# Performance work log

Measured on AMD Instinct MI355X. Metric: run time of the kernel, lower is better.

Reference implementation:

```python
import jax, jax.numpy as jnp
import numpy as np

N_NODES = 10000
N_EDGES = 160000
C = 16        # num_feature_channels
C2 = 8        # output channels per irrep per head (C/2)
HID = 64      # radial_network_hidden_units
NH = 2        # num_attention_heads
NG = 16       # graphs in batch
F_IN = 64     # num_features
F_OUT = 32    # number_of_output_features
HEAD_TYPES = ("normal", "inverse")  # invariant_dictionary
IRREP_SLICES = ((0, 1), (1, 4), (4, 9))  # l=0,1,2 blocks of the SH dim


def _sph_harm(r):
    """Component-normalized real spherical harmonics l=0..2 for unit vectors r [E,3] -> [E,9]."""
    x, y, z = r[:, 0], r[:, 1], r[:, 2]
    c3 = 1.7320508   # sqrt(3)
    c15 = 3.8729833  # sqrt(15)
    l0 = jnp.ones_like(x)[:, None]
    l1 = c3 * r
    l2 = jnp.stack([
        c15 * x * y,
        c15 * y * z,
        1.1180340 * (2.0 * z * z - x * x - y * y),  # sqrt(5)/2
        c15 * x * z,
        1.9364917 * (x * x - y * y),                 # sqrt(15)/2
    ], axis=-1)
    return jnp.concatenate([l0, l1, l2], axis=-1)


def setup_inputs() -> dict:
    key = jax.random.key(0)
    ks = jax.random.split(key, 16)
    node_features = jax.random.normal(ks[0], (N_NODES, F_IN), jnp.float32)
    pos = jax.random.normal(ks[1], (N_NODES, 3), jnp.float32)
    src = jax.random.randint(ks[2], (N_EDGES,), 0, N_NODES)
    off = jax.random.randint(ks[3], (N_EDGES,), 1, N_NODES)  # avoid self-loops (d=0)
    tgt = (src + off) % N_NODES
    edge_index = jnp.stack([src, tgt], axis=0)
    batch = jnp.sort(jax.random.randint(ks[4], (N_NODES,), 0, NG))
    s = lambda k, shape, fan: (jax.random.normal(k, shape, jnp.float32) / np.sqrt(fan)).astype(jnp.float32)
    return dict(
        node_features=node_features, pos=pos,
        W_embed=s(ks[5], (F_IN, C), F_IN), b_embed=jnp.zeros((C,), jnp.float32),
        Wq=s(ks[6], (NH, C, C), C), Wk=s(ks[7], (NH, C, C), C),
        W1=s(ks[8], (NH, 1, HID), 1), b1=jnp.zeros((NH, HID), jnp.float32),
        Wa=s(ks[9], (NH, HID), HID), Wv=s(ks[10], (NH, HID, C * 3), HID),
        Wo=s(ks[11], (NH, 3, C, C2), C),
        Wproj=s(ks[12], (NH * C2, F_OUT), NH * C2), bproj=jnp.zeros((F_OUT,), jnp.float32),
        edge_index=edge_index, batch=batch,
    )


def _forward(node_features, pos, W_embed, b_embed, Wq, Wk, W1, b1, Wa, Wv, Wo,
             Wproj, bproj, edge_index, batch):
    src, tgt = edge_index[0], edge_index[1]
    rel = pos[tgt] - pos[src]                       # [E,3]
    dist = jnp.linalg.norm(rel, axis=-1, keepdims=True)  # [E,1]
    rhat = rel / dist
    Y = _sph_harm(rhat)                             # [E,9]
    x = node_features @ W_embed + b_embed          # [N,C] scalar (0e) features
    xs = x[src]                                     # [E,C]
    inv_sqrt_c = 1.0 / np.sqrt(C)
    head_outs = []
    for h in range(NH):
        d_feat = dist if HEAD_TYPES[h] == "normal" else dist ** -2  # [E,1]
        hid = jax.nn.relu(d_feat @ W1[h] + b1[h])   # [E,HID] radial network
        att_bias = hid @ Wa[h]                      # [E]
        wv = (hid @ Wv[h]).reshape(-1, C, 3)        # [E,C,3] per-(channel,l) radial weights
        q = x @ Wq[h]
        k = x @ Wk[h]
        logit = jnp.sum(q[tgt] * k[src], axis=-1) * inv_sqrt_c + att_bias  # [E]
        # segment softmax over incoming edges of each target node
        m = jax.ops.segment_max(logit, tgt, num_segments=N_NODES)
        e = jnp.exp(logit - m[tgt])
        z = jax.ops.segment_sum(e, tgt, num_segments=N_NODES)
        alpha = e / z[tgt]                          # [E]
        # expand per-l weights to per-m: dims (1,3,5)
        wv_m = jnp.repeat(wv, np.array([1, 3, 5]), axis=2, total_repeat_length=9)  # [E,C,9]
        msg = (alpha[:, None, None] * wv_m) * xs[:, :, None] * Y[:, None, :]       # [E,C,9]
        node_out = jax.ops.segment_sum(msg, tgt, num_segments=N_NODES)             # [N,C,9]
        parts = [jnp.einsum('ncm,co->nom', node_out[:, :, s0:s1], Wo[h, li]).reshape(N_NODES, -1)
                 for li, (s0, s1) in enumerate(IRREP_SLICES)]
        head_outs.append(jnp.concatenate(parts, axis=-1))  # [N, C2*9]
    feat = jnp.concatenate(head_outs, axis=-1)              # [N, NH*C2*9]
    pooled = jax.ops.segment_sum(feat, batch, num_segments=NG)  # [NG, NH*C2*9]
    # equivariant Linear -> F_OUT x 0e: only scalar (l=0) components map to scalars
    blk = C2 * 9
    scal = jnp.concatenate([pooled[:, h * blk: h * blk + C2] for h in range(NH)], axis=-1)  # [NG, NH*C2]
    return scal @ Wproj + bproj                             # [NG, F_OUT]


def reference(node_features, pos, W_embed, b_embed, Wq, Wk, W1, b1, Wa, Wv, Wo,
              Wproj, bproj, edge_index, batch):
    return _forward(node_features, pos, W_embed, b_embed, Wq, Wk, W1, b1, Wa, Wv,
                    Wo, Wproj, bproj, edge_index, batch)
```

## Files before the change

### kernel.cpp

```cpp
#include <hip/hip_runtime.h>
#include <math.h>

#define NN 10000
#define NE 160000
#define CAP 96

__global__ __launch_bounds__(256) void k_xqk(const float* __restrict__ nf,
        const float* __restrict__ We, const float* __restrict__ be,
        const float* __restrict__ Wq, const float* __restrict__ Wk,
        float* __restrict__ x, float* __restrict__ q, float* __restrict__ k,
        int* __restrict__ zeroReg) {
    int t = threadIdx.x;
    int gid = blockIdx.x * 256 + t;
    if (gid < 10256) zeroReg[gid] = 0;
    __shared__ float sWe[64 * 16];
    __shared__ float sWq[2 * 16 * 16];
    __shared__ float sWk[2 * 16 * 16];
    __shared__ float sNF[16 * 64];
    __shared__ float sX[16 * 16];
    for (int i = t; i < 1024; i += 256) sWe[i] = We[i];
    for (int i = t; i < 512; i += 256) { sWq[i] = Wq[i]; sWk[i] = Wk[i]; }
    int nodeBase = blockIdx.x * 16;
    for (int i = t; i < 1024; i += 256) {
        int n = nodeBase + (i >> 6);
        sNF[i] = (n < NN) ? nf[n * 64 + (i & 63)] : 0.0f;
    }
    __syncthreads();
    int ln = t >> 4, c = t & 15;
    int n = nodeBase + ln;
    float acc = be[c];
    #pragma unroll 16
    for (int j = 0; j < 64; ++j) acc = fmaf(sNF[ln * 64 + j], sWe[j * 16 + c], acc);
    sX[ln * 16 + c] = acc;
    __syncthreads();
    if (n < NN) {
        x[n * 16 + c] = acc;
        #pragma unroll
        for (int h = 0; h < 2; ++h) {
            float aq = 0.0f, ak = 0.0f;
            #pragma unroll
            for (int j = 0; j < 16; ++j) {
                float xv = sX[ln * 16 + j];
                aq = fmaf(xv, sWq[(h * 16 + j) * 16 + c], aq);
                ak = fmaf(xv, sWk[(h * 16 + j) * 16 + c], ak);
            }
            q[(n * 2 + h) * 16 + c] = aq;
            k[(n * 2 + h) * 16 + c] = ak;
        }
    }
}

__global__ __launch_bounds__(256) void k_edge(const float* __restrict__ pos,
        const int* __restrict__ ei,
        const float* __restrict__ q, const float* __restrict__ k,
        const float* __restrict__ W1, const float* __restrict__ b1,
        const float* __restrict__ Wa, const float* __restrict__ Wv,
        const float* __restrict__ x, int* __restrict__ deg,
        float* __restrict__ lgp, float* __restrict__ wxs) {
    __shared__ float sW1[128], sB1[128], sWa[128];
    __shared__ float sV[2048];
    int t0 = threadIdx.x;
    if (t0 < 128) { sW1[t0] = W1[t0]; sB1[t0] = b1[t0]; sWa[t0] = Wa[t0]; }
    for (int i = t0; i < 2048; i += 256) {
        int h = i >> 10, j = (i >> 4) & 63, c = i & 15;
        sV[i] = Wv[(h * 64 + j) * 48 + 3 * c];
    }
    __syncthreads();
    int e = blockIdx.x * 256 + t0;
    if (e >= NE) return;
    int s = ei[e], t = ei[NE + e];
    int p = atomicAdd(&deg[t], 1);
    bool ok = (p < CAP);
    size_t slot = (size_t)t * CAP + p;
    float dx = pos[t * 3 + 0] - pos[s * 3 + 0];
    float dy = pos[t * 3 + 1] - pos[s * 3 + 1];
    float dz = pos[t * 3 + 2] - pos[s * 3 + 2];
    float d = sqrtf(dx * dx + dy * dy + dz * dz);
    float fh[2] = { d, 1.0f / (d * d) };
    const float4* qt = (const float4*)(q + (size_t)t * 32);
    const float4* ks = (const float4*)(k + (size_t)s * 32);
    const float4* xp = (const float4*)(x + (size_t)s * 16);
    float4 xs[4] = { xp[0], xp[1], xp[2], xp[3] };
    float L2v[2];
    float4* wp = (float4*)(wxs + slot * 32);
    #pragma unroll
    for (int h = 0; h < 2; ++h) {
        float4 a0 = qt[h * 4 + 0], a1 = qt[h * 4 + 1], a2 = qt[h * 4 + 2], a3 = qt[h * 4 + 3];
        float4 b0 = ks[h * 4 + 0], c1 = ks[h * 4 + 1], c2 = ks[h * 4 + 2], c3 = ks[h * 4 + 3];
        float dot = a0.x * b0.x + a0.y * b0.y + a0.z * b0.z + a0.w * b0.w
                  + a1.x * c1.x + a1.y * c1.y + a1.z * c1.z + a1.w * c1.w
                  + a2.x * c2.x + a2.y * c2.y + a2.z * c2.z + a2.w * c2.w
                  + a3.x * c3.x + a3.y * c3.y + a3.z * c3.z + a3.w * c3.w;
        float f = fh[h];
        float att = 0.0f;
        float acc[16];
        #pragma unroll
        for (int c = 0; c < 16; ++c) acc[c] = 0.0f;
        const float4* vp = (const float4*)(sV + h * 1024);
        for (int j = 0; j < 64; ++j) {
            float hj = fmaxf(fmaf(f, sW1[h * 64 + j], sB1[h * 64 + j]), 0.0f);
            att = fmaf(hj, sWa[h * 64 + j], att);
            float4 v0 = vp[j * 4 + 0], v1 = vp[j * 4 + 1], v2 = vp[j * 4 + 2], v3 = vp[j * 4 + 3];
            acc[0]  = fmaf(hj, v0.x, acc[0]);  acc[1]  = fmaf(hj, v0.y, acc[1]);
            acc[2]  = fmaf(hj, v0.z, acc[2]);  acc[3]  = fmaf(hj, v0.w, acc[3]);
            acc[4]  = fmaf(hj, v1.x, acc[4]);  acc[5]  = fmaf(hj, v1.y, acc[5]);
            acc[6]  = fmaf(hj, v1.z, acc[6]);  acc[7]  = fmaf(hj, v1.w, acc[7]);
            acc[8]  = fmaf(hj, v2.x, acc[8]);  acc[9]  = fmaf(hj, v2.y, acc[9]);
            acc[10] = fmaf(hj, v2.z, acc[10]); acc[11] = fmaf(hj, v2.w, acc[11]);
            acc[12] = fmaf(hj, v3.x, acc[12]); acc[13] = fmaf(hj, v3.y, acc[13]);
            acc[14] = fmaf(hj, v3.z, acc[14]); acc[15] = fmaf(hj, v3.w, acc[15]);
        }
        L2v[h] = fmaf(dot, 0.25f, att);
        if (ok) {
            wp[h * 4 + 0] = make_float4(acc[0] * xs[0].x, acc[1] * xs[0].y, acc[2] * xs[0].z, acc[3] * xs[0].w);
            wp[h * 4 + 1] = make_float4(acc[4] * xs[1].x, acc[5] * xs[1].y, acc[6] * xs[1].z, acc[7] * xs[1].w);
            wp[h * 4 + 2] = make_float4(acc[8] * xs[2].x, acc[9] * xs[2].y, acc[10] * xs[2].z, acc[11] * xs[2].w);
            wp[h * 4 + 3] = make_float4(acc[12] * xs[3].x, acc[13] * xs[3].y, acc[14] * xs[3].z, acc[15] * xs[3].w);
        }
    }
    if (ok) *(float2*)(lgp + slot * 2) = make_float2(L2v[0], L2v[1]);
}

__global__ __launch_bounds__(256) void k_gather(const int* __restrict__ deg,
        const float* __restrict__ lgp, const float* __restrict__ wxs,
        const float* __restrict__ Wo, float* __restrict__ feat) {
    __shared__ float sWo[256];
    __shared__ float sUn[4][16];
    int t0 = threadIdx.x;
    sWo[t0] = Wo[(t0 >> 7) * 384 + (t0 & 127)];
    __syncthreads();
    int wv = t0 >> 6;
    int lane = t0 & 63;
    int pid = blockIdx.x * 4 + wv;
    int n = pid >> 1, h = pid & 1;
    int dg = min(deg[n], CAP);
    int g = lane >> 4, c = lane & 15;
    float m = -INFINITY, z = 0.0f, u = 0.0f;
    const float* lgb = lgp + (size_t)n * (CAP * 2) + h;
    const float* wxb = wxs + (size_t)n * (CAP * 32) + h * 16 + c;
    for (int i = g; i < dg; i += 4) {
        float L  = lgb[i * 2];
        float wx = wxb[(size_t)i * 32];
        float nm = fmaxf(m, L);
        float sc = __expf(m - nm);
        float w  = __expf(L - nm);
        u = fmaf(u, sc, w * wx);
        z = fmaf(z, sc, w);
        m = nm;
    }
    #pragma unroll
    for (int off = 16; off <= 32; off <<= 1) {
        float mo = __shfl_xor(m, off, 64);
        float zo = __shfl_xor(z, off, 64);
        float uo = __shfl_xor(u, off, 64);
        float nm = fmaxf(m, mo);
        float a = __expf(m - nm), b = __expf(mo - nm);
        u = u * a + uo * b;
        z = z * a + zo * b;
        m = nm;
    }
    float un = (z > 0.0f) ? u / z : 0.0f;
    sUn[wv][c] = un;
    if (lane < 8) {
        float o_acc = 0.0f;
        #pragma unroll
        for (int cc = 0; cc < 16; ++cc)
            o_acc = fmaf(sUn[wv][cc], sWo[h * 128 + cc * 8 + lane], o_acc);
        feat[n * 16 + h * 8 + lane] = o_acc;
    }
}

__global__ __launch_bounds__(256) void k_pool(const float* __restrict__ feat,
        const int* __restrict__ batch, float* __restrict__ pooled) {
    __shared__ float sP[256];
    int t = threadIdx.x;
    sP[t] = 0.0f;
    __syncthreads();
    for (int i = blockIdx.x * 256 + t; i < NN * 16; i += 40 * 256) {
        int n = i >> 4, c = i & 15;
        atomicAdd(&sP[batch[n] * 16 + c], feat[i]);
    }
    __syncthreads();
    atomicAdd(&pooled[t], sP[t]);
}

__global__ __launch_bounds__(512) void k_final(const float* __restrict__ pooled,
        const float* __restrict__ Wproj, const float* __restrict__ bproj,
        float* __restrict__ out) {
    int t = threadIdx.x;
    int g = t >> 5, fo = t & 31;
    float acc = bproj[fo];
    #pragma unroll
    for (int j = 0; j < 16; ++j) acc = fmaf(pooled[g * 16 + j], Wproj[j * 32 + fo], acc);
    out[g * 32 + fo] = acc;
}

extern "C" void kernel_launch(void* const* d_in, const int* in_sizes, int n_in,
                              void* d_out, int out_size, void* d_ws, size_t ws_size,
                              hipStream_t stream) {
    const float* nf    = (const float*)d_in[0];
    const float* pos   = (const float*)d_in[1];
    const float* We    = (const float*)d_in[2];
    const float* be    = (const float*)d_in[3];
    const float* Wq    = (const float*)d_in[4];
    const float* Wk    = (const float*)d_in[5];
    const float* W1    = (const float*)d_in[6];
    const float* b1    = (const float*)d_in[7];
    const float* Wa    = (const float*)d_in[8];
    const float* Wv    = (const float*)d_in[9];
    const float* Wo    = (const float*)d_in[10];
    const float* Wproj = (const float*)d_in[11];
    const float* bproj = (const float*)d_in[12];
    const int*   ei    = (const int*)d_in[13];
    const int*   batch = (const int*)d_in[14];
    float* out = (float*)d_out;
    (void)in_sizes; (void)n_in; (void)out_size; (void)ws_size;

    float* ws     = (float*)d_ws;
    float* x      = ws;
    float* q      = x + 160000;
    float* k      = q + 320000;
    float* feat   = k + 320000;
    float* pooled = feat + 160000;
    int*   deg    = (int*)(pooled + 256);
    float* lgp    = (float*)(deg + 10000);
    float* wxs    = lgp + (size_t)NN * CAP * 2;

    hipLaunchKernelGGL(k_xqk,    dim3(625),  dim3(256), 0, stream, nf, We, be, Wq, Wk, x, q, k, (int*)pooled);
    hipLaunchKernelGGL(k_edge,   dim3(625),  dim3(256), 0, stream, pos, ei, q, k, W1, b1, Wa, Wv, x, deg, lgp, wxs);
    hipLaunchKernelGGL(k_gather, dim3(5000), dim3(256), 0, stream, deg, lgp, wxs, Wo, feat);
    hipLaunchKernelGGL(k_pool,   dim3(40),   dim3(256), 0, stream, feat, batch, pooled);
    hipLaunchKernelGGL(k_final,  dim3(1),    dim3(512), 0, stream, pooled, Wproj, bproj, out);
}
```

Measured before the change: 139.7 us.

## Apply Wo projection per edge before softmax gather to halve scattered payload

Because Wo is linear, it is applied to each edge's weighted value vector in the edge kernel, so each slot stores 8 projected values per head instead of 16. The gather kernel then reads half as much data and skips its shared-memory Wo step. The Wv column extraction moves into a precompute in the first kernel, and the edge kernel now reads weights from global memory instead of shared memory. This trades extra per-edge FMAs and uncached-in-LDS weight loads for lower memory traffic, and adds -inf guards in the online softmax.

```diff
diff --git a/kernel.cpp b/kernel.cpp
--- a/kernel.cpp
+++ b/kernel.cpp
@@ -8,11 +8,18 @@
 __global__ __launch_bounds__(256) void k_xqk(const float* __restrict__ nf,
         const float* __restrict__ We, const float* __restrict__ be,
         const float* __restrict__ Wq, const float* __restrict__ Wk,
+        const float* __restrict__ Wv,
         float* __restrict__ x, float* __restrict__ q, float* __restrict__ k,
-        int* __restrict__ zeroReg) {
+        int* __restrict__ zeroReg, float* __restrict__ vC) {
     int t = threadIdx.x;
     int gid = blockIdx.x * 256 + t;
     if (gid < 10256) zeroReg[gid] = 0;
+    if (blockIdx.x == 0) {
+        for (int i = t; i < 2048; i += 256) {
+            int h = i >> 10, j = (i >> 4) & 63, c = i & 15;
+            vC[i] = Wv[(h * 64 + j) * 48 + 3 * c];
+        }
+    }
     __shared__ float sWe[64 * 16];
     __shared__ float sWq[2 * 16 * 16];
     __shared__ float sWk[2 * 16 * 16];
@@ -54,19 +61,11 @@
         const int* __restrict__ ei,
         const float* __restrict__ q, const float* __restrict__ k,
         const float* __restrict__ W1, const float* __restrict__ b1,
-        const float* __restrict__ Wa, const float* __restrict__ Wv,
+        const float* __restrict__ Wa, const float* __restrict__ vC,
+        const float* __restrict__ Wo,
         const float* __restrict__ x, int* __restrict__ deg,
-        float* __restrict__ lgp, float* __restrict__ wxs) {
-    __shared__ float sW1[128], sB1[128], sWa[128];
-    __shared__ float sV[2048];
-    int t0 = threadIdx.x;
-    if (t0 < 128) { sW1[t0] = W1[t0]; sB1[t0] = b1[t0]; sWa[t0] = Wa[t0]; }
-    for (int i = t0; i < 2048; i += 256) {
-        int h = i >> 10, j = (i >> 4) & 63, c = i & 15;
-        sV[i] = Wv[(h * 64 + j) * 48 + 3 * c];
-    }
-    __syncthreads();
-    int e = blockIdx.x * 256 + t0;
+        float* __restrict__ lgp, float* __restrict__ gws) {
+    int e = blockIdx.x * 256 + threadIdx.x;
     if (e >= NE) return;
     int s = ei[e], t = ei[NE + e];
     int p = atomicAdd(&deg[t], 1);
@@ -77,16 +76,17 @@
     float dz = pos[t * 3 + 2] - pos[s * 3 + 2];
     float d = sqrtf(dx * dx + dy * dy + dz * dz);
     float fh[2] = { d, 1.0f / (d * d) };
-    const float4* qt = (const float4*)(q + (size_t)t * 32);
-    const float4* ks = (const float4*)(k + (size_t)s * 32);
     const float4* xp = (const float4*)(x + (size_t)s * 16);
-    float4 xs[4] = { xp[0], xp[1], xp[2], xp[3] };
+    float4 xs0 = xp[0], xs1 = xp[1], xs2 = xp[2], xs3 = xp[3];
+    float xf[16] = { xs0.x, xs0.y, xs0.z, xs0.w, xs1.x, xs1.y, xs1.z, xs1.w,
+                     xs2.x, xs2.y, xs2.z, xs2.w, xs3.x, xs3.y, xs3.z, xs3.w };
     float L2v[2];
-    float4* wp = (float4*)(wxs + slot * 32);
     #pragma unroll
     for (int h = 0; h < 2; ++h) {
-        float4 a0 = qt[h * 4 + 0], a1 = qt[h * 4 + 1], a2 = qt[h * 4 + 2], a3 = qt[h * 4 + 3];
-        float4 b0 = ks[h * 4 + 0], c1 = ks[h * 4 + 1], c2 = ks[h * 4 + 2], c3 = ks[h * 4 + 3];
+        const float4* qt = (const float4*)(q + (size_t)t * 32 + h * 16);
+        const float4* ks = (const float4*)(k + (size_t)s * 32 + h * 16);
+        float4 a0 = qt[0], a1 = qt[1], a2 = qt[2], a3 = qt[3];
+        float4 b0 = ks[0], c1 = ks[1], c2 = ks[2], c3 = ks[3];
         float dot = a0.x * b0.x + a0.y * b0.y + a0.z * b0.z + a0.w * b0.w
                   + a1.x * c1.x + a1.y * c1.y + a1.z * c1.z + a1.w * c1.w
                   + a2.x * c2.x + a2.y * c2.y + a2.z * c2.z + a2.w * c2.w
@@ -96,78 +96,75 @@
         float acc[16];
         #pragma unroll
         for (int c = 0; c < 16; ++c) acc[c] = 0.0f;
-        const float4* vp = (const float4*)(sV + h * 1024);
+        const float* w1b = W1 + h * 64;
+        const float* b1b = b1 + h * 64;
+        const float* wab = Wa + h * 64;
+        const float* vcb = vC + h * 1024;
+        #pragma unroll 8
         for (int j = 0; j < 64; ++j) {
-            float hj = fmaxf(fmaf(f, sW1[h * 64 + j], sB1[h * 64 + j]), 0.0f);
-            att = fmaf(hj, sWa[h * 64 + j], att);
-            float4 v0 = vp[j * 4 + 0], v1 = vp[j * 4 + 1], v2 = vp[j * 4 + 2], v3 = vp[j * 4 + 3];
-            acc[0]  = fmaf(hj, v0.x, acc[0]);  acc[1]  = fmaf(hj, v0.y, acc[1]);
-            acc[2]  = fmaf(hj, v0.z, acc[2]);  acc[3]  = fmaf(hj, v0.w, acc[3]);
-            acc[4]  = fmaf(hj, v1.x, acc[4]);  acc[5]  = fmaf(hj, v1.y, acc[5]);
-            acc[6]  = fmaf(hj, v1.z, acc[6]);  acc[7]  = fmaf(hj, v1.w, acc[7]);
-            acc[8]  = fmaf(hj, v2.x, acc[8]);  acc[9]  = fmaf(hj, v2.y, acc[9]);
-            acc[10] = fmaf(hj, v2.z, acc[10]); acc[11] = fmaf(hj, v2.w, acc[11]);
-            acc[12] = fmaf(hj, v3.x, acc[12]); acc[13] = fmaf(hj, v3.y, acc[13]);
-            acc[14] = fmaf(hj, v3.z, acc[14]); acc[15] = fmaf(hj, v3.w, acc[15]);
+            float hid = fmaxf(fmaf(f, w1b[j], b1b[j]), 0.0f);
+            att = fmaf(hid, wab[j], att);
+            #pragma unroll
+            for (int c = 0; c < 16; ++c)
+                acc[c] = fmaf(hid, vcb[j * 16 + c], acc[c]);
         }
         L2v[h] = fmaf(dot, 0.25f, att);
+        float g[8];
+        #pragma unroll
+        for (int o = 0; o < 8; ++o) g[o] = 0.0f;
+        const float* wob = Wo + h * 384;
+        #pragma unroll
+        for (int c = 0; c < 16; ++c) {
+            float axc = acc[c] * xf[c];
+            #pragma unroll
+            for (int o = 0; o < 8; ++o) g[o] = fmaf(axc, wob[c * 8 + o], g[o]);
+        }
         if (ok) {
-            wp[h * 4 + 0] = make_float4(acc[0] * xs[0].x, acc[1] * xs[0].y, acc[2] * xs[0].z, acc[3] * xs[0].w);
-            wp[h * 4 + 1] = make_float4(acc[4] * xs[1].x, acc[5] * xs[1].y, acc[6] * xs[1].z, acc[7] * xs[1].w);
-            wp[h * 4 + 2] = make_float4(acc[8] * xs[2].x, acc[9] * xs[2].y, acc[10] * xs[2].z, acc[11] * xs[2].w);
-            wp[h * 4 + 3] = make_float4(acc[12] * xs[3].x, acc[13] * xs[3].y, acc[14] * xs[3].z, acc[15] * xs[3].w);
+            float4* gp = (float4*)(gws + slot * 16 + h * 8);
+            gp[0] = make_float4(g[0], g[1], g[2], g[3]);
+            gp[1] = make_float4(g[4], g[5], g[6], g[7]);
         }
     }
     if (ok) *(float2*)(lgp + slot * 2) = make_float2(L2v[0], L2v[1]);
 }
 
 __global__ __launch_bounds__(256) void k_gather(const int* __restrict__ deg,
-        const float* __restrict__ lgp, const float* __restrict__ wxs,
-        const float* __restrict__ Wo, float* __restrict__ feat) {
-    __shared__ float sWo[256];
-    __shared__ float sUn[4][16];
+        const float* __restrict__ lgp, const float* __restrict__ gws,
+        float* __restrict__ feat) {
     int t0 = threadIdx.x;
-    sWo[t0] = Wo[(t0 >> 7) * 384 + (t0 & 127)];
-    __syncthreads();
     int wv = t0 >> 6;
     int lane = t0 & 63;
     int pid = blockIdx.x * 4 + wv;
     int n = pid >> 1, h = pid & 1;
     int dg = min(deg[n], CAP);
-    int g = lane >> 4, c = lane & 15;
+    int g = lane >> 3, o = lane & 7;
     float m = -INFINITY, z = 0.0f, u = 0.0f;
     const float* lgb = lgp + (size_t)n * (CAP * 2) + h;
-    const float* wxb = wxs + (size_t)n * (CAP * 32) + h * 16 + c;
-    for (int i = g; i < dg; i += 4) {
+    const float* gwb = gws + (size_t)n * (CAP * 16) + h * 8 + o;
+    for (int i = g; i < dg; i += 8) {
         float L  = lgb[i * 2];
-        float wx = wxb[(size_t)i * 32];
+        float gv = gwb[(size_t)i * 16];
         float nm = fmaxf(m, L);
-        float sc = __expf(m - nm);
+        float sc = (m > -INFINITY) ? __expf(m - nm) : 0.0f;
         float w  = __expf(L - nm);
-        u = fmaf(u, sc, w * wx);
+        u = fmaf(u, sc, w * gv);
         z = fmaf(z, sc, w);
         m = nm;
     }
     #pragma unroll
-    for (int off = 16; off <= 32; off <<= 1) {
+    for (int off = 8; off <= 32; off <<= 1) {
         float mo = __shfl_xor(m, off, 64);
         float zo = __shfl_xor(z, off, 64);
         float uo = __shfl_xor(u, off, 64);
         float nm = fmaxf(m, mo);
-        float a = __expf(m - nm), b = __expf(mo - nm);
+        float a = (m  > -INFINITY) ? __expf(m  - nm) : 0.0f;
+        float b = (mo > -INFINITY) ? __expf(mo - nm) : 0.0f;
         u = u * a + uo * b;
         z = z * a + zo * b;
         m = nm;
     }
     float un = (z > 0.0f) ? u / z : 0.0f;
-    sUn[wv][c] = un;
-    if (lane < 8) {
-        float o_acc = 0.0f;
-        #pragma unroll
-        for (int cc = 0; cc < 16; ++cc)
-            o_acc = fmaf(sUn[wv][cc], sWo[h * 128 + cc * 8 + lane], o_acc);
-        feat[n * 16 + h * 8 + lane] = o_acc;
-    }
+    if (lane < 8) feat[n * 16 + h * 8 + o] = un;
 }
 
 __global__ __launch_bounds__(256) void k_pool(const float* __restrict__ feat,
@@ -223,12 +220,13 @@
     float* feat   = k + 320000;
     float* pooled = feat + 160000;
     int*   deg    = (int*)(pooled + 256);
-    float* lgp    = (float*)(deg + 10000);
-    float* wxs    = lgp + (size_t)NN * CAP * 2;
-
-    hipLaunchKernelGGL(k_xqk,    dim3(625),  dim3(256), 0, stream, nf, We, be, Wq, Wk, x, q, k, (int*)pooled);
-    hipLaunchKernelGGL(k_edge,   dim3(625),  dim3(256), 0, stream, pos, ei, q, k, W1, b1, Wa, Wv, x, deg, lgp, wxs);
-    hipLaunchKernelGGL(k_gather, dim3(5000), dim3(256), 0, stream, deg, lgp, wxs, Wo, feat);
+    float* vC     = (float*)(deg + 10000);
+    float* lgp    = vC + 2048;
+    float* gws    = lgp + (size_t)NN * CAP * 2;
+
+    hipLaunchKernelGGL(k_xqk,    dim3(625),  dim3(256), 0, stream, nf, We, be, Wq, Wk, Wv, x, q, k, (int*)pooled, vC);
+    hipLaunchKernelGGL(k_edge,   dim3(625),  dim3(256), 0, stream, pos, ei, q, k, W1, b1, Wa, vC, Wo, x, deg, lgp, gws);
+    hipLaunchKernelGGL(k_gather, dim3(5000), dim3(256), 0, stream, deg, lgp, gws, feat);
     hipLaunchKernelGGL(k_pool,   dim3(40),   dim3(256), 0, stream, feat, batch, pooled);
     hipLaunchKernelGGL(k_final,  dim3(1),    dim3(512), 0, stream, pooled, Wproj, bproj, out);
 }
```

New measurement: 133.0 us. 1.05x faster.
